# Optimization experiments

Measured on AMD Instinct MI355X. Metric: run time of the kernel, lower is better.

The kernel has to match this reference:

```python
import jax, jax.numpy as jnp
import numpy as np

B, L, D, H, FF = 8, 512, 1024, 16, 4096
HD = D // H
EPS = 1e-5

def ste_round(x):
    # straight-through rounding (QAT)
    return x + jax.lax.stop_gradient(jnp.round(x) - x)

def fq_act(x):
    # 8-bit asymmetric per-tensor fake quant with dynamic min/max observer
    lo = jnp.minimum(jnp.min(x), 0.0)
    hi = jnp.maximum(jnp.max(x), 0.0)
    scale = jax.lax.stop_gradient(jnp.maximum((hi - lo) / 255.0, 1e-8))
    zp = jax.lax.stop_gradient(jnp.round(-lo / scale))
    q = jnp.clip(ste_round(x / scale) + zp, 0.0, 255.0)
    return (q - zp) * scale

def fq_w(w):
    # 8-bit symmetric per-tensor fake quant for weights
    scale = jax.lax.stop_gradient(jnp.maximum(jnp.max(jnp.abs(w)) / 127.0, 1e-8))
    q = jnp.clip(ste_round(w / scale), -128.0, 127.0)
    return q * scale

def qlinear(x, w, b):
    # QuantizedLayer: fake-quant weight, linear, fake-quant output activation
    return fq_act(jnp.einsum('...i,oi->...o', x, fq_w(w)) + b)

def layer_norm(x, g, b):
    mu = jnp.mean(x, axis=-1, keepdims=True)
    var = jnp.mean(jnp.square(x - mu), axis=-1, keepdims=True)
    return (x - mu) * jax.lax.rsqrt(var + EPS) * g + b

def setup_inputs() -> dict:
    key = jax.random.key(0)
    ks = jax.random.split(key, 8)
    s = 0.02
    return {
        'x': jax.random.normal(ks[0], (B, L, D), jnp.float32),
        'ln1_g': jnp.ones((D,), jnp.float32), 'ln1_b': jnp.zeros((D,), jnp.float32),
        'wq': jax.random.normal(ks[1], (D, D), jnp.float32) * s, 'bq': jnp.zeros((D,), jnp.float32),
        'wk': jax.random.normal(ks[2], (D, D), jnp.float32) * s, 'bk': jnp.zeros((D,), jnp.float32),
        'wv': jax.random.normal(ks[3], (D, D), jnp.float32) * s, 'bv': jnp.zeros((D,), jnp.float32),
        'wo': jax.random.normal(ks[4], (D, D), jnp.float32) * s, 'bo': jnp.zeros((D,), jnp.float32),
        'ln2_g': jnp.ones((D,), jnp.float32), 'ln2_b': jnp.zeros((D,), jnp.float32),
        'w_fc': jax.random.normal(ks[5], (FF, D), jnp.float32) * s, 'b_fc': jnp.zeros((FF,), jnp.float32),
        'w_proj': jax.random.normal(ks[6], (D, FF), jnp.float32) * s, 'b_proj': jnp.zeros((D,), jnp.float32),
    }

def reference(x, ln1_g, ln1_b, wq, bq, wk, bk, wv, bv, wo, bo,
              ln2_g, ln2_b, w_fc, b_fc, w_proj, b_proj):
    # --- attention sub-block ---
    h = layer_norm(x, ln1_g, ln1_b)
    def heads(t):  # [B,L,D] -> [B,H,L,HD]
        return t.reshape(B, L, H, HD).transpose(0, 2, 1, 3)
    # QuantizedLayer output fq + post_act fake quant (applied twice, per source)
    q = fq_act(heads(qlinear(h, wq, bq)))
    k = fq_act(heads(qlinear(h, wk, bk)))
    v = fq_act(heads(qlinear(h, wv, bv)))
    scale = 1.0 / np.sqrt(HD).astype(np.float32)
    attn = jnp.einsum('bhld,bhmd->bhlm', q, k) * scale  # [B,H,L,L]
    attn = jax.nn.softmax(attn, axis=-1)
    attn = fq_act(attn)  # softmax post-act fake quant (dropout p=0 is identity)
    ctx = jnp.einsum('bhlm,bhmd->bhld', attn, v)
    ctx = ctx.transpose(0, 2, 1, 3).reshape(B, L, D)
    x = x + qlinear(ctx, wo, bo)
    # --- MLP sub-block ---
    h2 = layer_norm(x, ln2_g, ln2_b)
    h2 = qlinear(h2, w_fc, b_fc)
    h2 = jax.nn.gelu(h2, approximate=False)  # torch nn.GELU default (erf)
    x = x + qlinear(h2, w_proj, b_proj)
    return x
```

## Files before the change

### kernel.cpp

```cpp
#include <hip/hip_runtime.h>
#include <cmath>

#define BB 8
#define LL 512
#define DD 1024
#define HH 16
#define HDD 64
#define FFD 4096
#define MTOK (BB*LL)
#define EPSF 1e-5f
#define BK 64

typedef __attribute__((ext_vector_type(8))) short bf16x8;
typedef __attribute__((ext_vector_type(4))) float f32x4;


struct WSet {
  const float* w[6];
  unsigned short* q[6];
  int n4[6];
};

__device__ inline void atomicMaxPos(float* addr, float v) {
  atomicMax((unsigned int*)addr, __float_as_uint(v));
}

__device__ inline unsigned short f2bf(float x) {
  unsigned int u = __float_as_uint(x);
  u += 0x7fffu + ((u >> 16) & 1u);
  return (unsigned short)(u >> 16);
}
__device__ inline float bf2f(unsigned short h) {
  return __uint_as_float((unsigned int)h << 16);
}

__device__ __forceinline__ void gld16(const unsigned short* g, unsigned short* l) {
  __builtin_amdgcn_global_load_lds(
      (const __attribute__((address_space(1))) unsigned int*)g,
      (__attribute__((address_space(3))) unsigned int*)l, 16, 0, 0);
}

__global__ void k_init_bcat(float* __restrict__ s, const float* __restrict__ b0,
                            const float* __restrict__ b1, const float* __restrict__ b2,
                            float* __restrict__ dst) {
  int i = blockIdx.x * blockDim.x + threadIdx.x;
  if (i < 256) s[i] = 0.0f;
  if (i < 3072) dst[i] = i < 1024 ? b0[i] : (i < 2048 ? b1[i - 1024] : b2[i - 2048]);
}

__global__ void k_absmax6(WSet ws, float* __restrict__ scal) {
  const int id = blockIdx.y;
  const float4* w4 = (const float4*)ws.w[id];
  const int n4 = ws.n4[id];
  float m = 0.0f;
  for (int i = blockIdx.x * blockDim.x + threadIdx.x; i < n4; i += gridDim.x * blockDim.x) {
    float4 v = w4[i];
    m = fmaxf(m, fmaxf(fmaxf(fabsf(v.x), fabsf(v.y)), fmaxf(fabsf(v.z), fabsf(v.w))));
  }
  #pragma unroll
  for (int o = 32; o; o >>= 1) m = fmaxf(m, __shfl_down(m, o, 64));
  __shared__ float sb[4];
  int lane = threadIdx.x & 63, wid = threadIdx.x >> 6;
  if (lane == 0) sb[wid] = m;
  __syncthreads();
  if (threadIdx.x == 0) atomicMaxPos(scal + id, fmaxf(fmaxf(sb[0], sb[1]), fmaxf(sb[2], sb[3])));
}

__global__ void k_quantw6(WSet ws, const float* __restrict__ scal) {
  const int id = blockIdx.y;
  float s = fmaxf(scal[id] / 127.0f, 1e-8f);
  const float4* w4 = (const float4*)ws.w[id];
  ushort4* q4 = (ushort4*)ws.q[id];
  const int n4 = ws.n4[id];
  for (int i = blockIdx.x * blockDim.x + threadIdx.x; i < n4; i += gridDim.x * blockDim.x) {
    float4 v = w4[i];
    ushort4 o;
    o.x = f2bf(fminf(fmaxf(rintf(v.x / s), -128.0f), 127.0f));
    o.y = f2bf(fminf(fmaxf(rintf(v.y / s), -128.0f), 127.0f));
    o.z = f2bf(fminf(fmaxf(rintf(v.z / s), -128.0f), 127.0f));
    o.w = f2bf(fminf(fmaxf(rintf(v.w / s), -128.0f), 127.0f));
    q4[i] = o;
  }
}

__device__ inline float2 fq_params(const float* sHi, const float* sNeg) {
  float hi = *sHi, lo = -(*sNeg);
  float scale = fmaxf((hi - lo) / 255.0f, 1e-8f);
  float zp = rintf(-lo / scale);
  return make_float2(scale, zp);
}
__device__ inline float fq1(float x, float scale, float zp) {
  float q = fminf(fmaxf(rintf(x / scale) + zp, 0.0f), 255.0f);
  return (q - zp) * scale;
}
__device__ inline float2 fq_params2(const float* sHi, const float* sNeg) {
  float2 p1 = fq_params(sHi, sNeg);
  float hi2 = fq1(*sHi, p1.x, p1.y);
  float lo2 = fq1(-(*sNeg), p1.x, p1.y);
  float scale = fmaxf((hi2 - lo2) / 255.0f, 1e-8f);
  float zp = rintf(-lo2 / scale);
  return make_float2(scale, zp);
}
__device__ inline float code2(float x, float2 p1, float2 p2) {
  float v1 = fq1(x, p1.x, p1.y);
  float q = fminf(fmaxf(rintf(v1 / p2.x) + p2.y, 0.0f), 255.0f);
  return q - p2.y;
}

__global__ void k_quant_codes(const float* __restrict__ src, int colBase,
                              unsigned short* __restrict__ oc, const float* __restrict__ sl) {
  float2 p1 = fq_params(sl, sl + 1);
  float2 p2 = fq_params2(sl, sl + 1);
  const int n4 = MTOK * DD / 4;
  for (int i = blockIdx.x * blockDim.x + threadIdx.x; i < n4; i += gridDim.x * blockDim.x) {
    int row = i >> 8, c = (i & 255) * 4;
    float4 v = *(const float4*)(src + (size_t)row * 3072 + colBase + c);
    ushort4 o;
    o.x = f2bf(code2(v.x, p1, p2)); o.y = f2bf(code2(v.y, p1, p2));
    o.z = f2bf(code2(v.z, p1, p2)); o.w = f2bf(code2(v.w, p1, p2));
    *(ushort4*)&oc[(size_t)row * DD + c] = o;
  }
}

__global__ __launch_bounds__(256) void k_quant_codes_vt(
    const float* __restrict__ src, unsigned short* __restrict__ vt,
    const float* __restrict__ sl) {
  __shared__ unsigned short tile[64 * 68];
  float2 p1 = fq_params(sl, sl + 1);
  float2 p2 = fq_params2(sl, sl + 1);
  const int m0 = blockIdx.x * 64, h = blockIdx.y, b = blockIdx.z;
  const int t = threadIdx.x;
  const int r = t >> 2, c0 = (t & 3) * 16;
  const float* s4 = src + ((size_t)(b * LL + m0 + r)) * 3072 + 2048 + h * HDD + c0;
  #pragma unroll
  for (int i = 0; i < 4; ++i) {
    float4 v = *(const float4*)(s4 + i * 4);
    ushort4 o;
    o.x = f2bf(code2(v.x, p1, p2)); o.y = f2bf(code2(v.y, p1, p2));
    o.z = f2bf(code2(v.z, p1, p2)); o.w = f2bf(code2(v.w, p1, p2));
    *(ushort4*)&tile[r * 68 + c0 + i * 4] = o;
  }
  __syncthreads();
  const int dr = t >> 2, ms = (t & 3) * 16;
  unsigned short* dst = vt + ((size_t)((b * HH + h) * HDD + dr)) * LL + m0 + ms;
  #pragma unroll
  for (int i = 0; i < 4; ++i) {
    ushort4 o;
    o.x = tile[(ms + i * 4 + 0) * 68 + dr];
    o.y = tile[(ms + i * 4 + 1) * 68 + dr];
    o.z = tile[(ms + i * 4 + 2) * 68 + dr];
    o.w = tile[(ms + i * 4 + 3) * 68 + dr];
    *(ushort4*)(dst + i * 4) = o;
  }
}

__global__ void k_sum_minmax(const float* __restrict__ parts, size_t pstride4, int np,
                             const float* __restrict__ bias, int n4, int cmask,
                             float* __restrict__ sl) {
  float hi = 0.0f, ng = 0.0f;
  for (int i = blockIdx.x * blockDim.x + threadIdx.x; i < n4; i += gridDim.x * blockDim.x) {
    float4 bc = *(const float4*)(bias + (i & cmask) * 4);
    float vx = bc.x, vy = bc.y, vz = bc.z, vw = bc.w;
    for (int j = 0; j < np; ++j) {
      float4 a = ((const float4*)parts)[j * pstride4 + i];
      vx += a.x; vy += a.y; vz += a.z; vw += a.w;
    }
    hi = fmaxf(hi, fmaxf(fmaxf(vx, vy), fmaxf(vz, vw)));
    ng = fmaxf(ng, fmaxf(fmaxf(-vx, -vy), fmaxf(-vz, -vw)));
  }
  #pragma unroll
  for (int o = 32; o; o >>= 1) {
    hi = fmaxf(hi, __shfl_down(hi, o, 64));
    ng = fmaxf(ng, __shfl_down(ng, o, 64));
  }
  __shared__ float sh[4], sn[4];
  int lane = threadIdx.x & 63, wid = threadIdx.x >> 6;
  if (lane == 0) { sh[wid] = hi; sn[wid] = ng; }
  __syncthreads();
  if (threadIdx.x == 0) {
    atomicMaxPos(sl, fmaxf(fmaxf(sh[0], sh[1]), fmaxf(sh[2], sh[3])));
    atomicMaxPos(sl + 1, fmaxf(fmaxf(sn[0], sn[1]), fmaxf(sn[2], sn[3])));
  }
}

__global__ void k_quant_res2(const float* __restrict__ parts, size_t pstride4, int np,
                             const float* __restrict__ bias, const float* __restrict__ res,
                             float* __restrict__ out, int n4, int cmask,
                             const float* __restrict__ sl) {
  float2 p = fq_params(sl, sl + 1);
  for (int i = blockIdx.x * blockDim.x + threadIdx.x; i < n4; i += gridDim.x * blockDim.x) {
    float4 bc = *(const float4*)(bias + (i & cmask) * 4);
    float vx = bc.x, vy = bc.y, vz = bc.z, vw = bc.w;
    for (int j = 0; j < np; ++j) {
      float4 a = ((const float4*)parts)[j * pstride4 + i];
      vx += a.x; vy += a.y; vz += a.z; vw += a.w;
    }
    float4 r = ((const float4*)res)[i];
    float4 o;
    o.x = r.x + fq1(vx, p.x, p.y);
    o.y = r.y + fq1(vy, p.x, p.y);
    o.z = r.z + fq1(vz, p.x, p.y);
    o.w = r.w + fq1(vw, p.x, p.y);
    ((float4*)out)[i] = o;
  }
}

__device__ inline float gelu_exact(float g) {
  return 0.5f * g * (1.0f + erff(g * 0.7071067811865475f));
}

__global__ void k_gelu_codes(const float* __restrict__ x,
                             unsigned short* __restrict__ ghi, unsigned short* __restrict__ glo,
                             int n4, const float* __restrict__ sl) {
  float2 p = fq_params(sl, sl + 1);
  for (int i = blockIdx.x * blockDim.x + threadIdx.x; i < n4; i += gridDim.x * blockDim.x) {
    float4 v = ((const float4*)x)[i];
    float g0 = gelu_exact(fq1(v.x, p.x, p.y)), g1 = gelu_exact(fq1(v.y, p.x, p.y));
    float g2 = gelu_exact(fq1(v.z, p.x, p.y)), g3 = gelu_exact(fq1(v.w, p.x, p.y));
    ushort4 h, l;
    h.x = f2bf(g0); l.x = f2bf(g0 - bf2f(h.x));
    h.y = f2bf(g1); l.y = f2bf(g1 - bf2f(h.y));
    h.z = f2bf(g2); l.z = f2bf(g2 - bf2f(h.z));
    h.w = f2bf(g3); l.w = f2bf(g3 - bf2f(h.w));
    ((ushort4*)ghi)[i] = h;
    ((ushort4*)glo)[i] = l;
  }
}

__device__ inline float block_sum256(float v, float* sb) {
  #pragma unroll
  for (int o = 32; o; o >>= 1) v += __shfl_down(v, o, 64);
  int lane = threadIdx.x & 63, wid = threadIdx.x >> 6;
  __syncthreads();
  if (lane == 0) sb[wid] = v;
  __syncthreads();
  return sb[0] + sb[1] + sb[2] + sb[3];
}

__global__ __launch_bounds__(256) void k_ln_bf(const float* __restrict__ x, const float* __restrict__ g,
                                               const float* __restrict__ bta,
                                               unsigned short* __restrict__ ohi,
                                               unsigned short* __restrict__ olo) {
  __shared__ float sb[4];
  int row = blockIdx.x;
  const float4* xr = (const float4*)(x + (size_t)row * DD);
  float4 v = xr[threadIdx.x];
  float mu = block_sum256(v.x + v.y + v.z + v.w, sb) * (1.0f / DD);
  float dx = v.x - mu, dy = v.y - mu, dz = v.z - mu, dw = v.w - mu;
  float var = block_sum256(dx*dx + dy*dy + dz*dz + dw*dw, sb) * (1.0f / DD);
  float rs = 1.0f / sqrtf(var + EPSF);
  float4 gv = ((const float4*)g)[threadIdx.x];
  float4 bv = ((const float4*)bta)[threadIdx.x];
  float o0 = dx * rs * gv.x + bv.x;
  float o1 = dy * rs * gv.y + bv.y;
  float o2 = dz * rs * gv.z + bv.z;
  float o3 = dw * rs * gv.w + bv.w;
  ushort4 h, l;
  h.x = f2bf(o0); l.x = f2bf(o0 - bf2f(h.x));
  h.y = f2bf(o1); l.y = f2bf(o1 - bf2f(h.y));
  h.z = f2bf(o2); l.z = f2bf(o2 - bf2f(h.z));
  h.w = f2bf(o3); l.w = f2bf(o3 - bf2f(h.w));
  ((ushort4*)(ohi + (size_t)row * DD))[threadIdx.x] = h;
  ((ushort4*)(olo + (size_t)row * DD))[threadIdx.x] = l;
}

__global__ __launch_bounds__(256) void k_res_ln(
    const float* __restrict__ parts, size_t pstride4,
    const float* __restrict__ bias, const float* __restrict__ res,
    float* __restrict__ x1, const float* __restrict__ sl,
    const float* __restrict__ g, const float* __restrict__ bta,
    unsigned short* __restrict__ ohi, unsigned short* __restrict__ olo) {
  __shared__ float sb[4];
  float2 p = fq_params(sl, sl + 1);
  int row = blockIdx.x, t = threadIdx.x;
  size_t i4 = (size_t)row * 256 + t;
  float4 a = ((const float4*)parts)[i4];
  float4 b = ((const float4*)parts)[pstride4 + i4];
  float4 bc = ((const float4*)bias)[t];
  float4 r = ((const float4*)res)[i4];
  float4 xv;
  xv.x = r.x + fq1(a.x + b.x + bc.x, p.x, p.y);
  xv.y = r.y + fq1(a.y + b.y + bc.y, p.x, p.y);
  xv.z = r.z + fq1(a.z + b.z + bc.z, p.x, p.y);
  xv.w = r.w + fq1(a.w + b.w + bc.w, p.x, p.y);
  ((float4*)x1)[i4] = xv;
  float mu = block_sum256(xv.x + xv.y + xv.z + xv.w, sb) * (1.0f / DD);
  float dx = xv.x - mu, dy = xv.y - mu, dz = xv.z - mu, dw = xv.w - mu;
  float var = block_sum256(dx*dx + dy*dy + dz*dz + dw*dw, sb) * (1.0f / DD);
  float rs = 1.0f / sqrtf(var + EPSF);
  float4 gv = ((const float4*)g)[t];
  float4 bv = ((const float4*)bta)[t];
  float o0 = dx * rs * gv.x + bv.x;
  float o1 = dy * rs * gv.y + bv.y;
  float o2 = dz * rs * gv.z + bv.z;
  float o3 = dw * rs * gv.w + bv.w;
  ushort4 h, l;
  h.x = f2bf(o0); l.x = f2bf(o0 - bf2f(h.x));
  h.y = f2bf(o1); l.y = f2bf(o1 - bf2f(h.y));
  h.z = f2bf(o2); l.z = f2bf(o2 - bf2f(h.z));
  h.w = f2bf(o3); l.w = f2bf(o3 - bf2f(h.w));
  ((ushort4*)(ohi + (size_t)row * DD))[t] = h;
  ((ushort4*)(olo + (size_t)row * DD))[t] = l;
}

__global__ __launch_bounds__(256, 3) void k_gemm_bf(
    const unsigned short* __restrict__ Ahi, const unsigned short* __restrict__ Alo,
    const unsigned short* __restrict__ Bq,
    const float* __restrict__ bias, const float* __restrict__ wsc, float* __restrict__ obs,
    float* __restrict__ C, int ldC, int K, int kLen, int segShift, size_t partStride) {
  __shared__ unsigned short sAh[128 * BK];
  __shared__ unsigned short sAl[128 * BK];
  __shared__ unsigned short sB [128 * BK];
  __shared__ float redH, redN;
  const int t = threadIdx.x;
  const int row0 = blockIdx.x * 128, col0 = blockIdx.y * 128;
  const int kOff = blockIdx.z * kLen;
  float* Cp = C + (size_t)blockIdx.z * partStride;
  const int wave = t >> 6, lane = t & 63;
  const int wr = (wave >> 1) * 64, wc = (wave & 1) * 64;
  const int fr = lane & 15, fq = lane >> 4;
  const int seg = col0 >> segShift;
  const float s = fmaxf(wsc[seg] / 127.0f, 1e-8f);
  if (t == 0) { redH = 0.f; redN = 0.f; }

  f32x4 acc[4][4];
  #pragma unroll
  for (int i = 0; i < 4; ++i)
    #pragma unroll
    for (int j = 0; j < 4; ++j) acc[i][j] = (f32x4){0.f, 0.f, 0.f, 0.f};

  const int srB = lane >> 3;
  const int scs = lane & 7;

  for (int k0 = kOff; k0 < kOff + kLen; k0 += BK) {
    __syncthreads();
    #pragma unroll
    for (int it = 0; it < 4; ++it) {
      int r = (wave * 4 + it) * 8 + srB;
      int g = scs ^ (r & 7);
      size_t ga = (size_t)(row0 + r) * K + k0 + g * 8;
      size_t gb = (size_t)(col0 + r) * K + k0 + g * 8;
      int ld = r * BK + scs * 8;
      gld16(Ahi + ga, &sAh[ld]);
      gld16(Alo + ga, &sAl[ld]);
      gld16(Bq + gb, &sB[ld]);
    }
    __syncthreads();
    #pragma unroll
    for (int hh = 0; hh < 2; ++hh) {
      bf16x8 ah[4], al[4], bb[4];
      #pragma unroll
      for (int i = 0; i < 4; ++i) {
        int Ra = wr + i * 16 + fr;
        int Rb = wc + i * 16 + fr;
        int ca = ((hh * 4 + fq) ^ (Ra & 7)) * 8;
        int cb = ((hh * 4 + fq) ^ (Rb & 7)) * 8;
        ah[i] = *(const bf16x8*)&sAh[Ra * BK + ca];
        al[i] = *(const bf16x8*)&sAl[Ra * BK + ca];
        bb[i] = *(const bf16x8*)&sB [Rb * BK + cb];
      }
      #pragma unroll
      for (int i = 0; i < 4; ++i)
        #pragma unroll
        for (int j = 0; j < 4; ++j) {
          acc[i][j] = __builtin_amdgcn_mfma_f32_16x16x32_bf16(ah[i], bb[j], acc[i][j], 0, 0, 0);
          acc[i][j] = __builtin_amdgcn_mfma_f32_16x16x32_bf16(al[i], bb[j], acc[i][j], 0, 0, 0);
        }
    }
  }

  float ohi = 0.f, ong = 0.f;
  #pragma unroll
  for (int i = 0; i < 4; ++i) {
    #pragma unroll
    for (int j = 0; j < 4; ++j) {
      int col = col0 + wc + j * 16 + fr;
      float bcol = bias ? bias[col] : 0.0f;
      #pragma unroll
      for (int rg = 0; rg < 4; ++rg) {
        int row = row0 + wr + i * 16 + fq * 4 + rg;
        float val = acc[i][j][rg] * s + bcol;
        if (obs) { ohi = fmaxf(ohi, val); ong = fmaxf(ong, -val); }
        Cp[(size_t)row * ldC + col] = val;
      }
    }
  }
  if (obs) {
    #pragma unroll
    for (int o = 32; o; o >>= 1) {
      ohi = fmaxf(ohi, __shfl_down(ohi, o, 64));
      ong = fmaxf(ong, __shfl_down(ong, o, 64));
    }
    if (lane == 0) { atomicMaxPos(&redH, ohi); atomicMaxPos(&redN, ong); }
    __syncthreads();
    if (t == 0) {
      atomicMaxPos(obs + 2 * seg, redH);
      atomicMaxPos(obs + 2 * seg + 1, redN);
    }
  }
}

__global__ __launch_bounds__(256, 2) void k_gemm_wide(
    const unsigned short* __restrict__ Ahi, const unsigned short* __restrict__ Alo,
    const unsigned short* __restrict__ Bq,
    const float* __restrict__ bias, const float* __restrict__ wsc, float* __restrict__ obs,
    float* __restrict__ C, int ldC, int K, int kLen, int segShift, size_t partStride) {
  __shared__ unsigned short sAh[128 * BK];
  __shared__ unsigned short sAl[128 * BK];
  __shared__ unsigned short sB [256 * BK];
  __shared__ float redH, redN;
  const int t = threadIdx.x;
  const int row0 = blockIdx.x * 128, col0 = blockIdx.y * 256;
  const int kOff = blockIdx.z * kLen;
  float* Cp = C + (size_t)blockIdx.z * partStride;
  const int wave = t >> 6, lane = t & 63;
  const int wr = (wave >> 1) * 64, wc = (wave & 1) * 128;
  const int fr = lane & 15, fq = lane >> 4;
  const int seg = col0 >> segShift;
  const float s = fmaxf(wsc[seg] / 127.0f, 1e-8f);
  if (t == 0) { redH = 0.f; redN = 0.f; }

  f32x4 acc[4][8];
  #pragma unroll
  for (int i = 0; i < 4; ++i)
    #pragma unroll
    for (int j = 0; j < 8; ++j) acc[i][j] = (f32x4){0.f, 0.f, 0.f, 0.f};

  const int srB = lane >> 3;
  const int scs = lane & 7;

  for (int k0 = kOff; k0 < kOff + kLen; k0 += BK) {
    __syncthreads();
    #pragma unroll
    for (int it = 0; it < 4; ++it) {
      int r = (wave * 4 + it) * 8 + srB;
      int g = scs ^ (r & 7);
      size_t ga = (size_t)(row0 + r) * K + k0 + g * 8;
      int ld = r * BK + scs * 8;
      gld16(Ahi + ga, &sAh[ld]);
      gld16(Alo + ga, &sAl[ld]);
    }
    #pragma unroll
    for (int it = 0; it < 8; ++it) {
      int r = (wave * 8 + it) * 8 + srB;
      int g = scs ^ (r & 7);
      size_t gb = (size_t)(col0 + r) * K + k0 + g * 8;
      gld16(Bq + gb, &sB[r * BK + scs * 8]);
    }
    __syncthreads();
    #pragma unroll
    for (int hh = 0; hh < 2; ++hh) {
      bf16x8 ah[4], al[4], bb[8];
      #pragma unroll
      for (int i = 0; i < 4; ++i) {
        int Ra = wr + i * 16 + fr;
        int ca = ((hh * 4 + fq) ^ (Ra & 7)) * 8;
        ah[i] = *(const bf16x8*)&sAh[Ra * BK + ca];
        al[i] = *(const bf16x8*)&sAl[Ra * BK + ca];
      }
      #pragma unroll
      for (int j = 0; j < 8; ++j) {
        int Rb = wc + j * 16 + fr;
        int cb = ((hh * 4 + fq) ^ (Rb & 7)) * 8;
        bb[j] = *(const bf16x8*)&sB[Rb * BK + cb];
      }
      #pragma unroll
      for (int i = 0; i < 4; ++i)
        #pragma unroll
        for (int j = 0; j < 8; ++j) {
          acc[i][j] = __builtin_amdgcn_mfma_f32_16x16x32_bf16(ah[i], bb[j], acc[i][j], 0, 0, 0);
          acc[i][j] = __builtin_amdgcn_mfma_f32_16x16x32_bf16(al[i], bb[j], acc[i][j], 0, 0, 0);
        }
    }
  }

  float ohi = 0.f, ong = 0.f;
  #pragma unroll
  for (int i = 0; i < 4; ++i) {
    #pragma unroll
    for (int j = 0; j < 8; ++j) {
      int col = col0 + wc + j * 16 + fr;
      float bcol = bias ? bias[col] : 0.0f;
      #pragma unroll
      for (int rg = 0; rg < 4; ++rg) {
        int row = row0 + wr + i * 16 + fq * 4 + rg;
        float val = acc[i][j][rg] * s + bcol;
        if (obs) { ohi = fmaxf(ohi, val); ong = fmaxf(ong, -val); }
        Cp[(size_t)row * ldC + col] = val;
      }
    }
  }
  if (obs) {
    #pragma unroll
    for (int o = 32; o; o >>= 1) {
      ohi = fmaxf(ohi, __shfl_down(ohi, o, 64));
      ong = fmaxf(ong, __shfl_down(ong, o, 64));
    }
    if (lane == 0) { atomicMaxPos(&redH, ohi); atomicMaxPos(&redN, ong); }
    __syncthreads();
    if (t == 0) {
      atomicMaxPos(obs + 2 * seg, redH);
      atomicMaxPos(obs + 2 * seg + 1, redN);
    }
  }
}

__global__ __launch_bounds__(256) void k_attn_a_mfma(
    const unsigned short* __restrict__ qc, const unsigned short* __restrict__ kc,
    const float* __restrict__ slq, const float* __restrict__ slk,
    float* __restrict__ rowm, float* __restrict__ rowz, float* __restrict__ maxp) {
  __shared__ unsigned short ks[64 * 72];
  __shared__ float redp;
  const int t = threadIdx.x, wave = t >> 6, lane = t & 63;
  const int fr = lane & 15, fq = lane >> 4;
  const int l0 = blockIdx.x * 64, h = blockIdx.y, b = blockIdx.z;
  const float sfac = fq_params2(slq, slq + 1).x * fq_params2(slk, slk + 1).x * 0.125f;
  if (t == 0) redp = 0.f;
  const unsigned short* qrow = qc + ((size_t)(b * LL + l0 + wave * 16 + fr)) * DD + h * HDD;
  bf16x8 qa0 = *(const bf16x8*)(qrow + fq * 8);
  bf16x8 qa1 = *(const bf16x8*)(qrow + 32 + fq * 8);
  float mrun[4] = {-INFINITY, -INFINITY, -INFINITY, -INFINITY};
  float zrun[4] = {0.f, 0.f, 0.f, 0.f};
  for (int mc = 0; mc < LL; mc += 64) {
    __syncthreads();
    #pragma unroll
    for (int it = 0; it < 2; ++it) {
      int si = t + it * 256, r = si >> 3, c8 = (si & 7) * 8;
      *(bf16x8*)&ks[r * 72 + c8] =
          *(const bf16x8*)(kc + ((size_t)(b * LL + mc + r)) * DD + h * HDD + c8);
    }
    __syncthreads();
    float sv[4][4];
    #pragma unroll
    for (int j = 0; j < 4; ++j) {
      bf16x8 b0 = *(const bf16x8*)&ks[(j * 16 + fr) * 72 + fq * 8];
      bf16x8 b1 = *(const bf16x8*)&ks[(j * 16 + fr) * 72 + 32 + fq * 8];
      f32x4 sAcc = (f32x4){0.f, 0.f, 0.f, 0.f};
      sAcc = __builtin_amdgcn_mfma_f32_16x16x32_bf16(qa0, b0, sAcc, 0, 0, 0);
      sAcc = __builtin_amdgcn_mfma_f32_16x16x32_bf16(qa1, b1, sAcc, 0, 0, 0);
      #pragma unroll
      for (int rg = 0; rg < 4; ++rg) sv[j][rg] = sAcc[rg] * sfac;
    }
    #pragma unroll
    for (int rg = 0; rg < 4; ++rg) {
      float nm = mrun[rg];
      #pragma unroll
      for (int j = 0; j < 4; ++j) nm = fmaxf(nm, sv[j][rg]);
      float z = zrun[rg] * expf(mrun[rg] - nm);
      #pragma unroll
      for (int j = 0; j < 4; ++j) z += expf(sv[j][rg] - nm);
      zrun[rg] = z; mrun[rg] = nm;
    }
  }
  #pragma unroll
  for (int off = 1; off < 16; off <<= 1) {
    #pragma unroll
    for (int rg = 0; rg < 4; ++rg) {
      float om = __shfl_xor(mrun[rg], off, 64);
      float oz = __shfl_xor(zrun[rg], off, 64);
      float nm = fmaxf(mrun[rg], om);
      zrun[rg] = zrun[rg] * expf(mrun[rg] - nm) + oz * expf(om - nm);
      mrun[rg] = nm;
    }
  }
  if (fr == 0) {
    int rid = (b * HH + h) * LL + l0 + wave * 16 + fq * 4;
    float lmax = 0.f;
    #pragma unroll
    for (int rg = 0; rg < 4; ++rg) {
      rowm[rid + rg] = mrun[rg]; rowz[rid + rg] = zrun[rg];
      lmax = fmaxf(lmax, 1.0f / zrun[rg]);
    }
    atomicMaxPos(&redp, lmax);
  }
  __syncthreads();
  if (t == 0) atomicMaxPos(maxp, redp);
}

__global__ __launch_bounds__(256) void k_attn_b_mfma(
    const unsigned short* __restrict__ qc, const unsigned short* __restrict__ kc,
    const unsigned short* __restrict__ vt,
    const float* __restrict__ slq, const float* __restrict__ slk, const float* __restrict__ slv,
    const float* __restrict__ rowm, const float* __restrict__ rowz,
    const float* __restrict__ maxp,
    unsigned short* __restrict__ chi, unsigned short* __restrict__ clo) {
  __shared__ unsigned short ks[64 * 72];
  __shared__ unsigned short vs[64 * 72];
  __shared__ unsigned short ps[4][16 * 72];
  const int t = threadIdx.x, wave = t >> 6, lane = t & 63;
  const int fr = lane & 15, fq = lane >> 4;
  const int l0 = blockIdx.x * 64, h = blockIdx.y, b = blockIdx.z;
  const float sfac = fq_params2(slq, slq + 1).x * fq_params2(slk, slk + 1).x * 0.125f;
  const float sv2 = fq_params2(slv, slv + 1).x;
  const float pscale = fmaxf(maxp[0] / 255.0f, 1e-8f);
  const float ipscale = 1.0f / pscale;
  const int ridb = (b * HH + h) * LL + l0 + wave * 16 + fq * 4;
  float rm[4], rzi[4];
  #pragma unroll
  for (int rg = 0; rg < 4; ++rg) { rm[rg] = rowm[ridb + rg]; rzi[rg] = 1.0f / rowz[ridb + rg]; }
  const unsigned short* qrow = qc + ((size_t)(b * LL + l0 + wave * 16 + fr)) * DD + h * HDD;
  bf16x8 qa0 = *(const bf16x8*)(qrow + fq * 8);
  bf16x8 qa1 = *(const bf16x8*)(qrow + 32 + fq * 8);
  f32x4 acc[4];
  #pragma unroll
  for (int jd = 0; jd < 4; ++jd) acc[jd] = (f32x4){0.f, 0.f, 0.f, 0.f};

  for (int mc = 0; mc < LL; mc += 64) {
    __syncthreads();
    #pragma unroll
    for (int it = 0; it < 2; ++it) {
      int si = t + it * 256, r = si >> 3, c8 = (si & 7) * 8;
      *(bf16x8*)&ks[r * 72 + c8] =
          *(const bf16x8*)(kc + ((size_t)(b * LL + mc + r)) * DD + h * HDD + c8);
      *(bf16x8*)&vs[r * 72 + c8] =
          *(const bf16x8*)(vt + ((size_t)((b * HH + h) * HDD + r)) * LL + mc + c8);
    }
    __syncthreads();
    #pragma unroll
    for (int j = 0; j < 4; ++j) {
      bf16x8 b0 = *(const bf16x8*)&ks[(j * 16 + fr) * 72 + fq * 8];
      bf16x8 b1 = *(const bf16x8*)&ks[(j * 16 + fr) * 72 + 32 + fq * 8];
      f32x4 sAcc = (f32x4){0.f, 0.f, 0.f, 0.f};
      sAcc = __builtin_amdgcn_mfma_f32_16x16x32_bf16(qa0, b0, sAcc, 0, 0, 0);
      sAcc = __builtin_amdgcn_mfma_f32_16x16x32_bf16(qa1, b1, sAcc, 0, 0, 0);
      #pragma unroll
      for (int rg = 0; rg < 4; ++rg) {
        float p = expf(sAcc[rg] * sfac - rm[rg]) * rzi[rg];
        float q = fminf(fmaxf(rintf(p * ipscale), 0.0f), 255.0f);
        ps[wave][(fq * 4 + rg) * 72 + j * 16 + fr] = f2bf(q);
      }
    }
    __syncthreads();
    bf16x8 pa0 = *(const bf16x8*)&ps[wave][fr * 72 + fq * 8];
    bf16x8 pa1 = *(const bf16x8*)&ps[wave][fr * 72 + 32 + fq * 8];
    #pragma unroll
    for (int jd = 0; jd < 4; ++jd) {
      bf16x8 vb0 = *(const bf16x8*)&vs[(jd * 16 + fr) * 72 + fq * 8];
      bf16x8 vb1 = *(const bf16x8*)&vs[(jd * 16 + fr) * 72 + 32 + fq * 8];
      acc[jd] = __builtin_amdgcn_mfma_f32_16x16x32_bf16(pa0, vb0, acc[jd], 0, 0, 0);
      acc[jd] = __builtin_amdgcn_mfma_f32_16x16x32_bf16(pa1, vb1, acc[jd], 0, 0, 0);
    }
  }
  const float osc = pscale * sv2;
  #pragma unroll
  for (int jd = 0; jd < 4; ++jd)
    #pragma unroll
    for (int rg = 0; rg < 4; ++rg) {
      int row = l0 + wave * 16 + fq * 4 + rg;
      size_t cidx = ((size_t)(b * LL + row)) * DD + h * HDD + jd * 16 + fr;
      float val = acc[jd][rg] * osc;
      unsigned short hh = f2bf(val);
      chi[cidx] = hh;
      clo[cidx] = f2bf(val - bf2f(hh));
    }
}

extern "C" void kernel_launch(void* const* d_in, const int* in_sizes, int n_in,
                              void* d_out, int out_size, void* d_ws, size_t ws_size,
                              hipStream_t stream) {
  const float* x    = (const float*)d_in[0];
  const float* ln1g = (const float*)d_in[1];
  const float* ln1b = (const float*)d_in[2];
  const float* wq   = (const float*)d_in[3];
  const float* bq   = (const float*)d_in[4];
  const float* wk   = (const float*)d_in[5];
  const float* bk   = (const float*)d_in[6];
  const float* wv   = (const float*)d_in[7];
  const float* bv   = (const float*)d_in[8];
  const float* wo   = (const float*)d_in[9];
  const float* bo   = (const float*)d_in[10];
  const float* ln2g = (const float*)d_in[11];
  const float* ln2b = (const float*)d_in[12];
  const float* wfc  = (const float*)d_in[13];
  const float* bfc  = (const float*)d_in[14];
  const float* wpj  = (const float*)d_in[15];
  const float* bpj  = (const float*)d_in[16];
  float* out = (float*)d_out;
  float* ws = (float*)d_ws;

  size_t off = 0;
  float* scal = ws + off; off += 256;
  float* bcat = ws + off; off += 3072;
  unsigned short* wcatQ = (unsigned short*)(ws + off); off += (size_t)3072*DD/2;
  unsigned short* woQ   = (unsigned short*)(ws + off); off += (size_t)DD*DD/2;
  unsigned short* wfcQ  = (unsigned short*)(ws + off); off += (size_t)FFD*DD/2;
  unsigned short* wpjQ  = (unsigned short*)(ws + off); off += (size_t)DD*FFD/2;
  unsigned short* abhi  = (unsigned short*)(ws + off); off += (size_t)MTOK*DD/2;
  unsigned short* ablo  = (unsigned short*)(ws + off); off += (size_t)MTOK*DD/2;
  float* qkvb = ws + off; off += (size_t)MTOK*3072;
  float* x1rg = ws + off; off += (size_t)MTOK*DD;
  unsigned short* vtc = (unsigned short*)(ws + off); off += (size_t)MTOK*DD/2;
  float* rowm = ws + off; off += (size_t)BB*HH*LL;
  float* rowz = ws + off; off += (size_t)BB*HH*LL;
  float* fcb  = ws + off; off += (size_t)MTOK*FFD;
  unsigned short* gello = (unsigned short*)(ws + off); off += (size_t)MTOK*FFD/2;

  unsigned short* qcod = (unsigned short*)x1rg;
  unsigned short* kcod = (unsigned short*)(x1rg + (size_t)MTOK*DD/2);
  float* x1 = x1rg;
  float* opart = qkvb;
  unsigned short* gelhi = (unsigned short*)qkvb;
  float* pjpart = fcb;

  const int ND  = MTOK*DD/4;
  const int NF  = MTOK*FFD/4;
  const int NW  = DD*DD/4;
  const int NWF = DD*FFD/4;
  const size_t PS4 = (size_t)MTOK*DD/4;

  auto g4 = [](int n4){ int g = (n4 + 255) / 256; return g > 4096 ? 4096 : g; };

  k_init_bcat<<<12, 256, 0, stream>>>(scal, bq, bk, bv, bcat);

  WSet wset;
  wset.w[0] = wq;  wset.q[0] = wcatQ;                   wset.n4[0] = NW;
  wset.w[1] = wk;  wset.q[1] = wcatQ + (size_t)DD*DD;   wset.n4[1] = NW;
  wset.w[2] = wv;  wset.q[2] = wcatQ + (size_t)2*DD*DD; wset.n4[2] = NW;
  wset.w[3] = wo;  wset.q[3] = woQ;                     wset.n4[3] = NW;
  wset.w[4] = wfc; wset.q[4] = wfcQ;                    wset.n4[4] = NWF;
  wset.w[5] = wpj; wset.q[5] = wpjQ;                    wset.n4[5] = NWF;

  k_absmax6<<<dim3(512, 6), 256, 0, stream>>>(wset, scal);
  k_quantw6<<<dim3(512, 6), 256, 0, stream>>>(wset, scal);

  k_ln_bf<<<MTOK, 256, 0, stream>>>(x, ln1g, ln1b, abhi, ablo);

  k_gemm_wide<<<dim3(32, 12, 1), 256, 0, stream>>>(abhi, ablo, wcatQ, bcat, scal+0, scal+6,
                                                   qkvb, 3072, DD, DD, 10, 0);

  k_quant_codes<<<g4(ND), 256, 0, stream>>>(qkvb, 0,    qcod, scal+6);
  k_quant_codes<<<g4(ND), 256, 0, stream>>>(qkvb, 1024, kcod, scal+8);
  k_quant_codes_vt<<<dim3(8, 16, 8), 256, 0, stream>>>(qkvb, vtc, scal+10);

  k_attn_a_mfma<<<dim3(8, 16, 8), 256, 0, stream>>>(qcod, kcod, scal+6, scal+8,
                                                    rowm, rowz, scal+18);
  k_attn_b_mfma<<<dim3(8, 16, 8), 256, 0, stream>>>(qcod, kcod, vtc, scal+6, scal+8, scal+10,
                                                    rowm, rowz, scal+18, abhi, ablo);

  k_gemm_bf<<<dim3(32, 8, 2), 256, 0, stream>>>(abhi, ablo, woQ, nullptr, scal+3, nullptr,
                                                opart, DD, DD, 512, 20, (size_t)MTOK*DD);
  k_sum_minmax<<<2048, 256, 0, stream>>>(opart, PS4, 2, bo, ND, 255, scal+19);
  k_res_ln<<<MTOK, 256, 0, stream>>>(opart, PS4, bo, x, x1, scal+19,
                                     ln2g, ln2b, abhi, ablo);

  k_gemm_wide<<<dim3(32, 16, 1), 256, 0, stream>>>(abhi, ablo, wfcQ, bfc, scal+4, scal+21,
                                                   fcb, FFD, DD, DD, 20, 0);
  k_gelu_codes<<<g4(NF), 256, 0, stream>>>(fcb, gelhi, gello, NF, scal+21);

  k_gemm_wide<<<dim3(32, 4, 4), 256, 0, stream>>>(gelhi, gello, wpjQ, nullptr, scal+5, nullptr,
                                                  pjpart, DD, FFD, 1024, 20, (size_t)MTOK*DD);
  k_sum_minmax<<<2048, 256, 0, stream>>>(pjpart, PS4, 4, bpj, ND, 255, scal+23);
  k_quant_res2<<<g4(ND), 256, 0, stream>>>(pjpart, PS4, 4, bpj, x1, out, ND, 255, scal+23);
}
```

Measured before the change: 621.7 us.

## Replace split bf16 hi/lo activations with single fp16 operands in all GEMMs

Switches every MFMA path from bf16 with a hi/lo split of activations (two MFMAs per tile) to a single fp16 operand using the f16 MFMA. The weight codes and attention integer codes are exact in fp16, so only one MFMA per tile and half the activation loads, stores and LDS are needed. The LayerNorm, context and GELU kernels now write one fp16 buffer, and the projection GEMM split-K drops from 4 to 2 partitions. The risk is fp16 rounding of activations (about 11-bit mantissa) and possible overflow, which could push borderline values across quantization bins.

```diff
diff --git a/kernel.cpp b/kernel.cpp
--- a/kernel.cpp
+++ b/kernel.cpp
@@ -11,7 +11,7 @@
 #define EPSF 1e-5f
 #define BK 64
 
-typedef __attribute__((ext_vector_type(8))) short bf16x8;
+typedef __attribute__((ext_vector_type(8))) _Float16 f16x8;
 typedef __attribute__((ext_vector_type(4))) float f32x4;
 
 
@@ -25,13 +25,10 @@
   atomicMax((unsigned int*)addr, __float_as_uint(v));
 }
 
-__device__ inline unsigned short f2bf(float x) {
-  unsigned int u = __float_as_uint(x);
-  u += 0x7fffu + ((u >> 16) & 1u);
-  return (unsigned short)(u >> 16);
-}
-__device__ inline float bf2f(unsigned short h) {
-  return __uint_as_float((unsigned int)h << 16);
+__device__ inline unsigned short f2h(float x) {
+  _Float16 h = (_Float16)x;
+  union { _Float16 hf; unsigned short u; } cv; cv.hf = h;
+  return cv.u;
 }
 
 __device__ __forceinline__ void gld16(const unsigned short* g, unsigned short* l) {
@@ -75,10 +72,10 @@
   for (int i = blockIdx.x * blockDim.x + threadIdx.x; i < n4; i += gridDim.x * blockDim.x) {
     float4 v = w4[i];
     ushort4 o;
-    o.x = f2bf(fminf(fmaxf(rintf(v.x / s), -128.0f), 127.0f));
-    o.y = f2bf(fminf(fmaxf(rintf(v.y / s), -128.0f), 127.0f));
-    o.z = f2bf(fminf(fmaxf(rintf(v.z / s), -128.0f), 127.0f));
-    o.w = f2bf(fminf(fmaxf(rintf(v.w / s), -128.0f), 127.0f));
+    o.x = f2h(fminf(fmaxf(rintf(v.x / s), -128.0f), 127.0f));
+    o.y = f2h(fminf(fmaxf(rintf(v.y / s), -128.0f), 127.0f));
+    o.z = f2h(fminf(fmaxf(rintf(v.z / s), -128.0f), 127.0f));
+    o.w = f2h(fminf(fmaxf(rintf(v.w / s), -128.0f), 127.0f));
     q4[i] = o;
   }
 }
@@ -116,8 +113,8 @@
     int row = i >> 8, c = (i & 255) * 4;
     float4 v = *(const float4*)(src + (size_t)row * 3072 + colBase + c);
     ushort4 o;
-    o.x = f2bf(code2(v.x, p1, p2)); o.y = f2bf(code2(v.y, p1, p2));
-    o.z = f2bf(code2(v.z, p1, p2)); o.w = f2bf(code2(v.w, p1, p2));
+    o.x = f2h(code2(v.x, p1, p2)); o.y = f2h(code2(v.y, p1, p2));
+    o.z = f2h(code2(v.z, p1, p2)); o.w = f2h(code2(v.w, p1, p2));
     *(ushort4*)&oc[(size_t)row * DD + c] = o;
   }
 }
@@ -136,8 +133,8 @@
   for (int i = 0; i < 4; ++i) {
     float4 v = *(const float4*)(s4 + i * 4);
     ushort4 o;
-    o.x = f2bf(code2(v.x, p1, p2)); o.y = f2bf(code2(v.y, p1, p2));
-    o.z = f2bf(code2(v.z, p1, p2)); o.w = f2bf(code2(v.w, p1, p2));
+    o.x = f2h(code2(v.x, p1, p2)); o.y = f2h(code2(v.y, p1, p2));
+    o.z = f2h(code2(v.z, p1, p2)); o.w = f2h(code2(v.w, p1, p2));
     *(ushort4*)&tile[r * 68 + c0 + i * 4] = o;
   }
   __syncthreads();
@@ -209,21 +206,17 @@
   return 0.5f * g * (1.0f + erff(g * 0.7071067811865475f));
 }
 
-__global__ void k_gelu_codes(const float* __restrict__ x,
-                             unsigned short* __restrict__ ghi, unsigned short* __restrict__ glo,
-                             int n4, const float* __restrict__ sl) {
+__global__ void k_gelu_h(const float* __restrict__ x, unsigned short* __restrict__ gh,
+                         int n4, const float* __restrict__ sl) {
   float2 p = fq_params(sl, sl + 1);
   for (int i = blockIdx.x * blockDim.x + threadIdx.x; i < n4; i += gridDim.x * blockDim.x) {
     float4 v = ((const float4*)x)[i];
-    float g0 = gelu_exact(fq1(v.x, p.x, p.y)), g1 = gelu_exact(fq1(v.y, p.x, p.y));
-    float g2 = gelu_exact(fq1(v.z, p.x, p.y)), g3 = gelu_exact(fq1(v.w, p.x, p.y));
-    ushort4 h, l;
-    h.x = f2bf(g0); l.x = f2bf(g0 - bf2f(h.x));
-    h.y = f2bf(g1); l.y = f2bf(g1 - bf2f(h.y));
-    h.z = f2bf(g2); l.z = f2bf(g2 - bf2f(h.z));
-    h.w = f2bf(g3); l.w = f2bf(g3 - bf2f(h.w));
-    ((ushort4*)ghi)[i] = h;
-    ((ushort4*)glo)[i] = l;
+    ushort4 h;
+    h.x = f2h(gelu_exact(fq1(v.x, p.x, p.y)));
+    h.y = f2h(gelu_exact(fq1(v.y, p.x, p.y)));
+    h.z = f2h(gelu_exact(fq1(v.z, p.x, p.y)));
+    h.w = f2h(gelu_exact(fq1(v.w, p.x, p.y)));
+    ((ushort4*)gh)[i] = h;
   }
 }
 
@@ -237,10 +230,9 @@
   return sb[0] + sb[1] + sb[2] + sb[3];
 }
 
-__global__ __launch_bounds__(256) void k_ln_bf(const float* __restrict__ x, const float* __restrict__ g,
-                                               const float* __restrict__ bta,
-                                               unsigned short* __restrict__ ohi,
-                                               unsigned short* __restrict__ olo) {
+__global__ __launch_bounds__(256) void k_ln_h(const float* __restrict__ x, const float* __restrict__ g,
+                                              const float* __restrict__ bta,
+                                              unsigned short* __restrict__ oh) {
   __shared__ float sb[4];
   int row = blockIdx.x;
   const float4* xr = (const float4*)(x + (size_t)row * DD);
@@ -251,17 +243,12 @@
   float rs = 1.0f / sqrtf(var + EPSF);
   float4 gv = ((const float4*)g)[threadIdx.x];
   float4 bv = ((const float4*)bta)[threadIdx.x];
-  float o0 = dx * rs * gv.x + bv.x;
-  float o1 = dy * rs * gv.y + bv.y;
-  float o2 = dz * rs * gv.z + bv.z;
-  float o3 = dw * rs * gv.w + bv.w;
-  ushort4 h, l;
-  h.x = f2bf(o0); l.x = f2bf(o0 - bf2f(h.x));
-  h.y = f2bf(o1); l.y = f2bf(o1 - bf2f(h.y));
-  h.z = f2bf(o2); l.z = f2bf(o2 - bf2f(h.z));
-  h.w = f2bf(o3); l.w = f2bf(o3 - bf2f(h.w));
-  ((ushort4*)(ohi + (size_t)row * DD))[threadIdx.x] = h;
-  ((ushort4*)(olo + (size_t)row * DD))[threadIdx.x] = l;
+  ushort4 h;
+  h.x = f2h(dx * rs * gv.x + bv.x);
+  h.y = f2h(dy * rs * gv.y + bv.y);
+  h.z = f2h(dz * rs * gv.z + bv.z);
+  h.w = f2h(dw * rs * gv.w + bv.w);
+  ((ushort4*)(oh + (size_t)row * DD))[threadIdx.x] = h;
 }
 
 __global__ __launch_bounds__(256) void k_res_ln(
@@ -269,7 +256,7 @@
     const float* __restrict__ bias, const float* __restrict__ res,
     float* __restrict__ x1, const float* __restrict__ sl,
     const float* __restrict__ g, const float* __restrict__ bta,
-    unsigned short* __restrict__ ohi, unsigned short* __restrict__ olo) {
+    unsigned short* __restrict__ oh) {
   __shared__ float sb[4];
   float2 p = fq_params(sl, sl + 1);
   int row = blockIdx.x, t = threadIdx.x;
@@ -290,27 +277,20 @@
   float rs = 1.0f / sqrtf(var + EPSF);
   float4 gv = ((const float4*)g)[t];
   float4 bv = ((const float4*)bta)[t];
-  float o0 = dx * rs * gv.x + bv.x;
-  float o1 = dy * rs * gv.y + bv.y;
-  float o2 = dz * rs * gv.z + bv.z;
-  float o3 = dw * rs * gv.w + bv.w;
-  ushort4 h, l;
-  h.x = f2bf(o0); l.x = f2bf(o0 - bf2f(h.x));
-  h.y = f2bf(o1); l.y = f2bf(o1 - bf2f(h.y));
-  h.z = f2bf(o2); l.z = f2bf(o2 - bf2f(h.z));
-  h.w = f2bf(o3); l.w = f2bf(o3 - bf2f(h.w));
-  ((ushort4*)(ohi + (size_t)row * DD))[t] = h;
-  ((ushort4*)(olo + (size_t)row * DD))[t] = l;
-}
-
-__global__ __launch_bounds__(256, 3) void k_gemm_bf(
-    const unsigned short* __restrict__ Ahi, const unsigned short* __restrict__ Alo,
-    const unsigned short* __restrict__ Bq,
+  ushort4 h;
+  h.x = f2h(dx * rs * gv.x + bv.x);
+  h.y = f2h(dy * rs * gv.y + bv.y);
+  h.z = f2h(dz * rs * gv.z + bv.z);
+  h.w = f2h(dw * rs * gv.w + bv.w);
+  ((ushort4*)(oh + (size_t)row * DD))[t] = h;
+}
+
+__global__ __launch_bounds__(256, 4) void k_gemm_h(
+    const unsigned short* __restrict__ Aq, const unsigned short* __restrict__ Bq,
     const float* __restrict__ bias, const float* __restrict__ wsc, float* __restrict__ obs,
     float* __restrict__ C, int ldC, int K, int kLen, int segShift, size_t partStride) {
-  __shared__ unsigned short sAh[128 * BK];
-  __shared__ unsigned short sAl[128 * BK];
-  __shared__ unsigned short sB [128 * BK];
+  __shared__ unsigned short sA[128 * BK];
+  __shared__ unsigned short sB[128 * BK];
   __shared__ float redH, redN;
   const int t = threadIdx.x;
   const int row0 = blockIdx.x * 128, col0 = blockIdx.y * 128;
@@ -341,31 +321,25 @@
       size_t ga = (size_t)(row0 + r) * K + k0 + g * 8;
       size_t gb = (size_t)(col0 + r) * K + k0 + g * 8;
       int ld = r * BK + scs * 8;
-      gld16(Ahi + ga, &sAh[ld]);
-      gld16(Alo + ga, &sAl[ld]);
+      gld16(Aq + ga, &sA[ld]);
       gld16(Bq + gb, &sB[ld]);
     }
     __syncthreads();
     #pragma unroll
     for (int hh = 0; hh < 2; ++hh) {
-      bf16x8 ah[4], al[4], bb[4];
+      f16x8 av[4], bb[4];
       #pragma unroll
       for (int i = 0; i < 4; ++i) {
         int Ra = wr + i * 16 + fr;
         int Rb = wc + i * 16 + fr;
-        int ca = ((hh * 4 + fq) ^ (Ra & 7)) * 8;
-        int cb = ((hh * 4 + fq) ^ (Rb & 7)) * 8;
-        ah[i] = *(const bf16x8*)&sAh[Ra * BK + ca];
-        al[i] = *(const bf16x8*)&sAl[Ra * BK + ca];
-        bb[i] = *(const bf16x8*)&sB [Rb * BK + cb];
+        av[i] = *(const f16x8*)&sA[Ra * BK + (((hh * 4 + fq) ^ (Ra & 7)) * 8)];
+        bb[i] = *(const f16x8*)&sB[Rb * BK + (((hh * 4 + fq) ^ (Rb & 7)) * 8)];
       }
       #pragma unroll
       for (int i = 0; i < 4; ++i)
         #pragma unroll
-        for (int j = 0; j < 4; ++j) {
-          acc[i][j] = __builtin_amdgcn_mfma_f32_16x16x32_bf16(ah[i], bb[j], acc[i][j], 0, 0, 0);
-          acc[i][j] = __builtin_amdgcn_mfma_f32_16x16x32_bf16(al[i], bb[j], acc[i][j], 0, 0, 0);
-        }
+        for (int j = 0; j < 4; ++j)
+          acc[i][j] = __builtin_amdgcn_mfma_f32_16x16x32_f16(av[i], bb[j], acc[i][j], 0, 0, 0);
     }
   }
 
@@ -401,13 +375,11 @@
 }
 
 __global__ __launch_bounds__(256, 2) void k_gemm_wide(
-    const unsigned short* __restrict__ Ahi, const unsigned short* __restrict__ Alo,
-    const unsigned short* __restrict__ Bq,
+    const unsigned short* __restrict__ Aq, const unsigned short* __restrict__ Bq,
     const float* __restrict__ bias, const float* __restrict__ wsc, float* __restrict__ obs,
     float* __restrict__ C, int ldC, int K, int kLen, int segShift, size_t partStride) {
-  __shared__ unsigned short sAh[128 * BK];
-  __shared__ unsigned short sAl[128 * BK];
-  __shared__ unsigned short sB [256 * BK];
+  __shared__ unsigned short sA[128 * BK];
+  __shared__ unsigned short sB[256 * BK];
   __shared__ float redH, redN;
   const int t = threadIdx.x;
   const int row0 = blockIdx.x * 128, col0 = blockIdx.y * 256;
@@ -436,9 +408,7 @@
       int r = (wave * 4 + it) * 8 + srB;
       int g = scs ^ (r & 7);
       size_t ga = (size_t)(row0 + r) * K + k0 + g * 8;
-      int ld = r * BK + scs * 8;
-      gld16(Ahi + ga, &sAh[ld]);
-      gld16(Alo + ga, &sAl[ld]);
+      gld16(Aq + ga, &sA[r * BK + scs * 8]);
     }
     #pragma unroll
     for (int it = 0; it < 8; ++it) {
@@ -450,27 +420,22 @@
     __syncthreads();
     #pragma unroll
     for (int hh = 0; hh < 2; ++hh) {
-      bf16x8 ah[4], al[4], bb[8];
+      f16x8 av[4], bb[8];
       #pragma unroll
       for (int i = 0; i < 4; ++i) {
         int Ra = wr + i * 16 + fr;
-        int ca = ((hh * 4 + fq) ^ (Ra & 7)) * 8;
-        ah[i] = *(const bf16x8*)&sAh[Ra * BK + ca];
-        al[i] = *(const bf16x8*)&sAl[Ra * BK + ca];
+        av[i] = *(const f16x8*)&sA[Ra * BK + (((hh * 4 + fq) ^ (Ra & 7)) * 8)];
       }
       #pragma unroll
       for (int j = 0; j < 8; ++j) {
         int Rb = wc + j * 16 + fr;
-        int cb = ((hh * 4 + fq) ^ (Rb & 7)) * 8;
-        bb[j] = *(const bf16x8*)&sB[Rb * BK + cb];
+        bb[j] = *(const f16x8*)&sB[Rb * BK + (((hh * 4 + fq) ^ (Rb & 7)) * 8)];
       }
       #pragma unroll
       for (int i = 0; i < 4; ++i)
         #pragma unroll
-        for (int j = 0; j < 8; ++j) {
-          acc[i][j] = __builtin_amdgcn_mfma_f32_16x16x32_bf16(ah[i], bb[j], acc[i][j], 0, 0, 0);
-          acc[i][j] = __builtin_amdgcn_mfma_f32_16x16x32_bf16(al[i], bb[j], acc[i][j], 0, 0, 0);
-        }
+        for (int j = 0; j < 8; ++j)
+          acc[i][j] = __builtin_amdgcn_mfma_f32_16x16x32_f16(av[i], bb[j], acc[i][j], 0, 0, 0);
     }
   }
 
@@ -517,8 +482,8 @@
   const float sfac = fq_params2(slq, slq + 1).x * fq_params2(slk, slk + 1).x * 0.125f;
   if (t == 0) redp = 0.f;
   const unsigned short* qrow = qc + ((size_t)(b * LL + l0 + wave * 16 + fr)) * DD + h * HDD;
-  bf16x8 qa0 = *(const bf16x8*)(qrow + fq * 8);
-  bf16x8 qa1 = *(const bf16x8*)(qrow + 32 + fq * 8);
+  f16x8 qa0 = *(const f16x8*)(qrow + fq * 8);
+  f16x8 qa1 = *(const f16x8*)(qrow + 32 + fq * 8);
   float mrun[4] = {-INFINITY, -INFINITY, -INFINITY, -INFINITY};
   float zrun[4] = {0.f, 0.f, 0.f, 0.f};
   for (int mc = 0; mc < LL; mc += 64) {
@@ -526,18 +491,18 @@
     #pragma unroll
     for (int it = 0; it < 2; ++it) {
       int si = t + it * 256, r = si >> 3, c8 = (si & 7) * 8;
-      *(bf16x8*)&ks[r * 72 + c8] =
-          *(const bf16x8*)(kc + ((size_t)(b * LL + mc + r)) * DD + h * HDD + c8);
+      *(f16x8*)&ks[r * 72 + c8] =
+          *(const f16x8*)(kc + ((size_t)(b * LL + mc + r)) * DD + h * HDD + c8);
     }
     __syncthreads();
     float sv[4][4];
     #pragma unroll
     for (int j = 0; j < 4; ++j) {
-      bf16x8 b0 = *(const bf16x8*)&ks[(j * 16 + fr) * 72 + fq * 8];
-      bf16x8 b1 = *(const bf16x8*)&ks[(j * 16 + fr) * 72 + 32 + fq * 8];
+      f16x8 b0 = *(const f16x8*)&ks[(j * 16 + fr) * 72 + fq * 8];
+      f16x8 b1 = *(const f16x8*)&ks[(j * 16 + fr) * 72 + 32 + fq * 8];
       f32x4 sAcc = (f32x4){0.f, 0.f, 0.f, 0.f};
-      sAcc = __builtin_amdgcn_mfma_f32_16x16x32_bf16(qa0, b0, sAcc, 0, 0, 0);
-      sAcc = __builtin_amdgcn_mfma_f32_16x16x32_bf16(qa1, b1, sAcc, 0, 0, 0);
+      sAcc = __builtin_amdgcn_mfma_f32_16x16x32_f16(qa0, b0, sAcc, 0, 0, 0);
+      sAcc = __builtin_amdgcn_mfma_f32_16x16x32_f16(qa1, b1, sAcc, 0, 0, 0);
       #pragma unroll
       for (int rg = 0; rg < 4; ++rg) sv[j][rg] = sAcc[rg] * sfac;
     }
@@ -582,8 +547,7 @@
     const unsigned short* __restrict__ vt,
     const float* __restrict__ slq, const float* __restrict__ slk, const float* __restrict__ slv,
     const float* __restrict__ rowm, const float* __restrict__ rowz,
-    const float* __restrict__ maxp,
-    unsigned short* __restrict__ chi, unsigned short* __restrict__ clo) {
+    const float* __restrict__ maxp, unsigned short* __restrict__ ch) {
   __shared__ unsigned short ks[64 * 72];
   __shared__ unsigned short vs[64 * 72];
   __shared__ unsigned short ps[4][16 * 72];
@@ -599,8 +563,8 @@
   #pragma unroll
   for (int rg = 0; rg < 4; ++rg) { rm[rg] = rowm[ridb + rg]; rzi[rg] = 1.0f / rowz[ridb + rg]; }
   const unsigned short* qrow = qc + ((size_t)(b * LL + l0 + wave * 16 + fr)) * DD + h * HDD;
-  bf16x8 qa0 = *(const bf16x8*)(qrow + fq * 8);
-  bf16x8 qa1 = *(const bf16x8*)(qrow + 32 + fq * 8);
+  f16x8 qa0 = *(const f16x8*)(qrow + fq * 8);
+  f16x8 qa1 = *(const f16x8*)(qrow + 32 + fq * 8);
   f32x4 acc[4];
   #pragma unroll
   for (int jd = 0; jd < 4; ++jd) acc[jd] = (f32x4){0.f, 0.f, 0.f, 0.f};
@@ -610,35 +574,35 @@
     #pragma unroll
     for (int it = 0; it < 2; ++it) {
       int si = t + it * 256, r = si >> 3, c8 = (si & 7) * 8;
-      *(bf16x8*)&ks[r * 72 + c8] =
-          *(const bf16x8*)(kc + ((size_t)(b * LL + mc + r)) * DD + h * HDD + c8);
-      *(bf16x8*)&vs[r * 72 + c8] =
-          *(const bf16x8*)(vt + ((size_t)((b * HH + h) * HDD + r)) * LL + mc + c8);
+      *(f16x8*)&ks[r * 72 + c8] =
+          *(const f16x8*)(kc + ((size_t)(b * LL + mc + r)) * DD + h * HDD + c8);
+      *(f16x8*)&vs[r * 72 + c8] =
+          *(const f16x8*)(vt + ((size_t)((b * HH + h) * HDD + r)) * LL + mc + c8);
     }
     __syncthreads();
     #pragma unroll
     for (int j = 0; j < 4; ++j) {
-      bf16x8 b0 = *(const bf16x8*)&ks[(j * 16 + fr) * 72 + fq * 8];
-      bf16x8 b1 = *(const bf16x8*)&ks[(j * 16 + fr) * 72 + 32 + fq * 8];
+      f16x8 b0 = *(const f16x8*)&ks[(j * 16 + fr) * 72 + fq * 8];
+      f16x8 b1 = *(const f16x8*)&ks[(j * 16 + fr) * 72 + 32 + fq * 8];
       f32x4 sAcc = (f32x4){0.f, 0.f, 0.f, 0.f};
-      sAcc = __builtin_amdgcn_mfma_f32_16x16x32_bf16(qa0, b0, sAcc, 0, 0, 0);
-      sAcc = __builtin_amdgcn_mfma_f32_16x16x32_bf16(qa1, b1, sAcc, 0, 0, 0);
+      sAcc = __builtin_amdgcn_mfma_f32_16x16x32_f16(qa0, b0, sAcc, 0, 0, 0);
+      sAcc = __builtin_amdgcn_mfma_f32_16x16x32_f16(qa1, b1, sAcc, 0, 0, 0);
       #pragma unroll
       for (int rg = 0; rg < 4; ++rg) {
         float p = expf(sAcc[rg] * sfac - rm[rg]) * rzi[rg];
         float q = fminf(fmaxf(rintf(p * ipscale), 0.0f), 255.0f);
-        ps[wave][(fq * 4 + rg) * 72 + j * 16 + fr] = f2bf(q);
+        ps[wave][(fq * 4 + rg) * 72 + j * 16 + fr] = f2h(q);
       }
     }
     __syncthreads();
-    bf16x8 pa0 = *(const bf16x8*)&ps[wave][fr * 72 + fq * 8];
-    bf16x8 pa1 = *(const bf16x8*)&ps[wave][fr * 72 + 32 + fq * 8];
+    f16x8 pa0 = *(const f16x8*)&ps[wave][fr * 72 + fq * 8];
+    f16x8 pa1 = *(const f16x8*)&ps[wave][fr * 72 + 32 + fq * 8];
     #pragma unroll
     for (int jd = 0; jd < 4; ++jd) {
-      bf16x8 vb0 = *(const bf16x8*)&vs[(jd * 16 + fr) * 72 + fq * 8];
-      bf16x8 vb1 = *(const bf16x8*)&vs[(jd * 16 + fr) * 72 + 32 + fq * 8];
-      acc[jd] = __builtin_amdgcn_mfma_f32_16x16x32_bf16(pa0, vb0, acc[jd], 0, 0, 0);
-      acc[jd] = __builtin_amdgcn_mfma_f32_16x16x32_bf16(pa1, vb1, acc[jd], 0, 0, 0);
+      f16x8 vb0 = *(const f16x8*)&vs[(jd * 16 + fr) * 72 + fq * 8];
+      f16x8 vb1 = *(const f16x8*)&vs[(jd * 16 + fr) * 72 + 32 + fq * 8];
+      acc[jd] = __builtin_amdgcn_mfma_f32_16x16x32_f16(pa0, vb0, acc[jd], 0, 0, 0);
+      acc[jd] = __builtin_amdgcn_mfma_f32_16x16x32_f16(pa1, vb1, acc[jd], 0, 0, 0);
     }
   }
   const float osc = pscale * sv2;
@@ -648,10 +612,7 @@
     for (int rg = 0; rg < 4; ++rg) {
       int row = l0 + wave * 16 + fq * 4 + rg;
       size_t cidx = ((size_t)(b * LL + row)) * DD + h * HDD + jd * 16 + fr;
-      float val = acc[jd][rg] * osc;
-      unsigned short hh = f2bf(val);
-      chi[cidx] = hh;
-      clo[cidx] = f2bf(val - bf2f(hh));
+      ch[cidx] = f2h(acc[jd][rg] * osc);
     }
 }
 
@@ -685,21 +646,19 @@
   unsigned short* woQ   = (unsigned short*)(ws + off); off += (size_t)DD*DD/2;
   unsigned short* wfcQ  = (unsigned short*)(ws + off); off += (size_t)FFD*DD/2;
   unsigned short* wpjQ  = (unsigned short*)(ws + off); off += (size_t)DD*FFD/2;
-  unsigned short* abhi  = (unsigned short*)(ws + off); off += (size_t)MTOK*DD/2;
-  unsigned short* ablo  = (unsigned short*)(ws + off); off += (size_t)MTOK*DD/2;
+  unsigned short* ah16  = (unsigned short*)(ws + off); off += (size_t)MTOK*DD/2;
   float* qkvb = ws + off; off += (size_t)MTOK*3072;
   float* x1rg = ws + off; off += (size_t)MTOK*DD;
   unsigned short* vtc = (unsigned short*)(ws + off); off += (size_t)MTOK*DD/2;
   float* rowm = ws + off; off += (size_t)BB*HH*LL;
   float* rowz = ws + off; off += (size_t)BB*HH*LL;
   float* fcb  = ws + off; off += (size_t)MTOK*FFD;
-  unsigned short* gello = (unsigned short*)(ws + off); off += (size_t)MTOK*FFD/2;
 
   unsigned short* qcod = (unsigned short*)x1rg;
   unsigned short* kcod = (unsigned short*)(x1rg + (size_t)MTOK*DD/2);
   float* x1 = x1rg;
   float* opart = qkvb;
-  unsigned short* gelhi = (unsigned short*)qkvb;
+  unsigned short* gelf = (unsigned short*)qkvb;
   float* pjpart = fcb;
 
   const int ND  = MTOK*DD/4;
@@ -723,9 +682,9 @@
   k_absmax6<<<dim3(512, 6), 256, 0, stream>>>(wset, scal);
   k_quantw6<<<dim3(512, 6), 256, 0, stream>>>(wset, scal);
 
-  k_ln_bf<<<MTOK, 256, 0, stream>>>(x, ln1g, ln1b, abhi, ablo);
-
-  k_gemm_wide<<<dim3(32, 12, 1), 256, 0, stream>>>(abhi, ablo, wcatQ, bcat, scal+0, scal+6,
+  k_ln_h<<<MTOK, 256, 0, stream>>>(x, ln1g, ln1b, ah16);
+
+  k_gemm_wide<<<dim3(32, 12, 1), 256, 0, stream>>>(ah16, wcatQ, bcat, scal+0, scal+6,
                                                    qkvb, 3072, DD, DD, 10, 0);
 
   k_quant_codes<<<g4(ND), 256, 0, stream>>>(qkvb, 0,    qcod, scal+6);
@@ -735,20 +694,20 @@
   k_attn_a_mfma<<<dim3(8, 16, 8), 256, 0, stream>>>(qcod, kcod, scal+6, scal+8,
                                                     rowm, rowz, scal+18);
   k_attn_b_mfma<<<dim3(8, 16, 8), 256, 0, stream>>>(qcod, kcod, vtc, scal+6, scal+8, scal+10,
-                                                    rowm, rowz, scal+18, abhi, ablo);
-
-  k_gemm_bf<<<dim3(32, 8, 2), 256, 0, stream>>>(abhi, ablo, woQ, nullptr, scal+3, nullptr,
-                                                opart, DD, DD, 512, 20, (size_t)MTOK*DD);
+                                                    rowm, rowz, scal+18, ah16);
+
+  k_gemm_h<<<dim3(32, 8, 2), 256, 0, stream>>>(ah16, woQ, nullptr, scal+3, nullptr,
+                                               opart, DD, DD, 512, 20, (size_t)MTOK*DD);
   k_sum_minmax<<<2048, 256, 0, stream>>>(opart, PS4, 2, bo, ND, 255, scal+19);
   k_res_ln<<<MTOK, 256, 0, stream>>>(opart, PS4, bo, x, x1, scal+19,
-                                     ln2g, ln2b, abhi, ablo);
-
-  k_gemm_wide<<<dim3(32, 16, 1), 256, 0, stream>>>(abhi, ablo, wfcQ, bfc, scal+4, scal+21,
+                                     ln2g, ln2b, ah16);
+
+  k_gemm_wide<<<dim3(32, 16, 1), 256, 0, stream>>>(ah16, wfcQ, bfc, scal+4, scal+21,
                                                    fcb, FFD, DD, DD, 20, 0);
-  k_gelu_codes<<<g4(NF), 256, 0, stream>>>(fcb, gelhi, gello, NF, scal+21);
-
-  k_gemm_wide<<<dim3(32, 4, 4), 256, 0, stream>>>(gelhi, gello, wpjQ, nullptr, scal+5, nullptr,
-                                                  pjpart, DD, FFD, 1024, 20, (size_t)MTOK*DD);
-  k_sum_minmax<<<2048, 256, 0, stream>>>(pjpart, PS4, 4, bpj, ND, 255, scal+23);
-  k_quant_res2<<<g4(ND), 256, 0, stream>>>(pjpart, PS4, 4, bpj, x1, out, ND, 255, scal+23);
-}
+  k_gelu_h<<<g4(NF), 256, 0, stream>>>(fcb, gelf, NF, scal+21);
+
+  k_gemm_wide<<<dim3(32, 4, 2), 256, 0, stream>>>(gelf, wpjQ, nullptr, scal+5, nullptr,
+                                                  pjpart, DD, FFD, 2048, 20, (size_t)MTOK*DD);
+  k_sum_minmax<<<2048, 256, 0, stream>>>(pjpart, PS4, 2, bpj, ND, 255, scal+23);
+  k_quant_res2<<<g4(ND), 256, 0, stream>>>(pjpart, PS4, 2, bpj, x1, out, ND, 255, scal+23);
+}
```

Result: faster. 573.7 us (-7.7%).
